# Kernel tuning notes

Hardware: AMD Instinct MI355X
Metric: run time of the kernel (lower is better)

The kernel has to match this reference:

```python
import jax, jax.numpy as jnp
import numpy as np

SUPPORT = 7
NEIGHBOR = 10
EPS = 1e-12
BN_EPS = 1e-5


def knn(v, k):
    # v: (b, n, 3) -> (b, n, k) indices of k nearest (excluding self)
    sq = jnp.sum(v * v, -1)
    d = sq[:, :, None] + sq[:, None, :] - 2.0 * jnp.einsum('bnd,bmd->bnm', v, v)
    _, idx = jax.lax.top_k(-d, k + 1)
    return idx[:, :, 1:]


def gather_nb(f, idx):
    # f: (b, n, c), idx: (b, m, k) -> (b, m, k, c)
    b = f.shape[0]
    return f[jnp.arange(b)[:, None, None], idx]


def nb_dir_norm(v, idx):
    d = gather_nb(v, idx) - v[:, :, None, :]
    n = jnp.linalg.norm(d, axis=-1, keepdims=True)
    return d / jnp.maximum(n, EPS)


def norm0(d):
    n = jnp.linalg.norm(d, axis=0, keepdims=True)
    return d / jnp.maximum(n, EPS)


def conv_surface(idx, v, directions, kernel_num):
    b, n, k = idx.shape
    dn = nb_dir_norm(v, idx)
    theta = jax.nn.relu(jnp.einsum('bnkd,de->bnke', dn, norm0(directions)))
    theta = theta.reshape(b, n, k, SUPPORT, kernel_num)
    return jnp.sum(jnp.max(theta, axis=2), axis=2)  # (b, n, kernel_num)


def conv_layer(idx, v, fmap, w, bias, directions, out_ch):
    b, n, k = idx.shape
    dn = nb_dir_norm(v, idx)
    theta = jax.nn.relu(jnp.einsum('bnkd,de->bnke', dn, norm0(directions)))  # (b,n,k,s*o)
    fout = fmap @ w + bias  # (b, n, (s+1)*o)
    center = fout[..., :out_ch]
    supp = gather_nb(fout[..., out_ch:], idx)  # (b, n, k, s*o)
    act = (theta * supp).reshape(b, n, k, SUPPORT, out_ch)
    return center + jnp.sum(jnp.max(act, axis=2), axis=2)


def pool(v, f, rate, nbn, seed):
    b, n, _ = v.shape
    idx = knn(v, nbn)
    pf = jnp.max(gather_nb(f, idx), axis=2)
    m = n // rate
    samp = jax.random.permutation(jax.random.key(seed), n)[:m]
    return v[:, samp, :], pf[:, samp, :]


def nearest_idx(tgt, src):
    d = (jnp.sum(src * src, -1)[:, None, :] + jnp.sum(tgt * tgt, -1)[:, :, None]
         - 2.0 * jnp.einsum('btd,bsd->bts', tgt, src))
    return jnp.argmin(d, axis=-1)  # (b, nt)


def bn(x, g, b_, m, var):
    # per-channel over last dim (torch BN1d after transpose)
    return (x - m) / jnp.sqrt(var + BN_EPS) * g + b_


def setup_inputs() -> dict:
    key = jax.random.key(0)
    ks = jax.random.split(key, 32)
    bs, n = 4, 2048
    d = {}
    d['vertices'] = jax.random.normal(ks[0], (bs, n, 3), jnp.float32)
    d['rgb_f'] = jax.random.normal(ks[1], (bs, 32, n), jnp.float32)
    d['dir0'] = jax.random.normal(ks[2], (3, SUPPORT * 64), jnp.float32)
    def conv_params(i, cin, cout):
        s = 1.0 / np.sqrt(cin)
        w = jax.random.uniform(ks[i], (cin, (SUPPORT + 1) * cout), jnp.float32, -s, s)
        b = jax.random.uniform(ks[i + 1], ((SUPPORT + 1) * cout,), jnp.float32, -s, s)
        dr = jax.random.normal(ks[i + 2], (3, SUPPORT * cout), jnp.float32)
        return w, b, dr
    d['w1'], d['b1'], d['d1'] = conv_params(3, 128, 128)
    d['w2'], d['b2'], d['d2'] = conv_params(6, 128, 256)
    d['w3'], d['b3'], d['d3'] = conv_params(9, 256, 256)
    d['w4'], d['b4'], d['d4'] = conv_params(12, 256, 512)
    d['rgb_w'] = jax.random.normal(ks[15], (64, 32), jnp.float32) * 0.1
    d['rgb_b'] = jnp.zeros((64,), jnp.float32)
    for nm, c in [('rbn', 64), ('bn1', 128), ('bn2', 256), ('bn3', 256)]:
        d[nm + '_g'] = jnp.ones((c,), jnp.float32)
        d[nm + '_b'] = jnp.zeros((c,), jnp.float32)
        d[nm + '_m'] = jnp.zeros((c,), jnp.float32)
        d[nm + '_v'] = jnp.ones((c,), jnp.float32)
    return d


def reference(vertices, rgb_f, dir0,
              w1, b1, d1, w2, b2, d2, w3, b3, d3, w4, b4, d4,
              rgb_w, rgb_b,
              rbn_g, rbn_b, rbn_m, rbn_v,
              bn1_g, bn1_b, bn1_m, bn1_v,
              bn2_g, bn2_b, bn2_m, bn2_v,
              bn3_g, bn3_b, bn3_m, bn3_v):
    bs, n, _ = vertices.shape
    idx = knn(vertices, NEIGHBOR)
    fm0 = jax.nn.relu(conv_surface(idx, vertices, dir0, 64))  # (b, n, 64)
    # rgb_conv_1: Conv1d(32,64,1) -> ReLU -> BN
    rgb = jax.nn.relu(jnp.einsum('oc,bcn->bno', rgb_w, rgb_f) + rgb_b)  # (b, n, 64)
    rgb = bn(rgb, rbn_g, rbn_b, rbn_m, rbn_v)
    fm0 = jnp.concatenate([fm0, rgb], axis=-1)  # (b, n, 128)
    fm1 = jax.nn.relu(bn(conv_layer(idx, vertices, fm0, w1, b1, d1, 128),
                         bn1_g, bn1_b, bn1_m, bn1_v))
    v1, fp1 = pool(vertices, fm1, 4, 4, 1)  # (b, n/4, ...)
    k1 = min(NEIGHBOR, v1.shape[1] // 8)
    idx1 = knn(v1, k1)
    fm2 = jax.nn.relu(bn(conv_layer(idx1, v1, fp1, w2, b2, d2, 256),
                         bn2_g, bn2_b, bn2_m, bn2_v))
    fm3 = jax.nn.relu(bn(conv_layer(idx1, v1, fm2, w3, b3, d3, 256),
                         bn3_g, bn3_b, bn3_m, bn3_v))
    v2, fp2 = pool(v1, fm3, 4, 4, 2)  # (b, n/16, ...)
    k2 = min(NEIGHBOR, v2.shape[1] // 8)
    idx2 = knn(v2, k2)
    fm4 = conv_layer(idx2, v2, fp2, w4, b4, d4, 512)
    f_global = jnp.max(fm4, axis=1)  # (b, 512)
    ni1 = nearest_idx(vertices, v1)  # (b, n)
    ni2 = nearest_idx(vertices, v2)
    ar = jnp.arange(bs)[:, None]
    fm2u = fm2[ar, ni1]
    fm3u = fm3[ar, ni1]
    fm4u = fm4[ar, ni2]
    feat = jnp.concatenate([fm0, fm1, fm2u, fm3u, fm4u], axis=2)  # (b, n, 1280)
    fuse = jnp.concatenate([feat, jnp.broadcast_to(f_global[:, None, :], (bs, n, 512))], axis=2)
    return feat.transpose(0, 2, 1), fuse.transpose(0, 2, 1)
```

## Files before the change

kernel.cpp:

```cpp
#include <hip/hip_runtime.h>
#include <hip/hip_bf16.h>
#include <math.h>

#define NB 10
#define KNN_K 11

typedef __attribute__((ext_vector_type(8))) short bf16x8;
typedef __attribute__((ext_vector_type(4))) float f32x4;

__device__ __forceinline__ float toF(float x) { return x; }
__device__ __forceinline__ float toF(__hip_bfloat16 x) { return __bfloat162float(x); }

__device__ __forceinline__ void tf2x32(unsigned k0, unsigned k1, unsigned& x0, unsigned& x1) {
  unsigned ks0 = k0, ks1 = k1, ks2 = k0 ^ k1 ^ 0x1BD11BDAu;
  x0 += ks0; x1 += ks1;
#define TF_R(r) { x0 += x1; x1 = (x1 << (r)) | (x1 >> (32 - (r))); x1 ^= x0; }
  TF_R(13) TF_R(15) TF_R(26) TF_R(6)  x0 += ks1; x1 += ks2 + 1u;
  TF_R(17) TF_R(29) TF_R(16) TF_R(24) x0 += ks2; x1 += ks0 + 2u;
  TF_R(13) TF_R(15) TF_R(26) TF_R(6)  x0 += ks0; x1 += ks1 + 3u;
  TF_R(17) TF_R(29) TF_R(16) TF_R(24) x0 += ks1; x1 += ks2 + 4u;
  TF_R(13) TF_R(15) TF_R(26) TF_R(6)  x0 += ks2; x1 += ks0 + 5u;
#undef TF_R
}

__device__ __forceinline__ unsigned long long shfl_xor_u64(unsigned long long v, int m) {
  unsigned lo = (unsigned)v, hi = (unsigned)(v >> 32);
  lo = (unsigned)__shfl_xor((int)lo, m);
  hi = (unsigned)__shfl_xor((int)hi, m);
  return ((unsigned long long)hi << 32) | lo;
}

__device__ __forceinline__ void knn_wave_body(const float4* __restrict__ pts, int N, int qi,
                                              int lane, int* __restrict__ o) {
  float4 p = pts[qi];
  float bd[KNN_K]; int bi[KNN_K];
#pragma unroll
  for (int t = 0; t < KNN_K; ++t) { bd[t] = 3.4e38f; bi[t] = 0x7fffffff; }
  for (int j = lane; j < N; j += 64) {
    float4 q = pts[j];
    float dot = p.x * q.x + p.y * q.y + p.z * q.z;
    float d = p.w + q.w - 2.0f * dot;
    if (d < bd[KNN_K - 1]) {
      float cd = d; int ci = j;
#pragma unroll
      for (int t = 0; t < KNN_K; ++t) {
        bool sw = cd < bd[t];
        float td = bd[t]; int ti = bi[t];
        bd[t] = sw ? cd : td; bi[t] = sw ? ci : ti;
        cd = sw ? td : cd;   ci = sw ? ti : ci;
      }
    }
  }
  int ptr = 0;
#pragma unroll 1
  for (int t = 0; t < KNN_K; ++t) {
    float d = 3.4e38f; int idx = 0x7fffffff;
#pragma unroll
    for (int s = 0; s < KNN_K; ++s) {
      bool sel = (s == ptr);
      d = sel ? bd[s] : d;
      idx = sel ? bi[s] : idx;
    }
    float rd = d; int ridx = idx;
#pragma unroll
    for (int s = 32; s > 0; s >>= 1) {
      float od = __shfl_xor(rd, s);
      int oi = __shfl_xor(ridx, s);
      if (od < rd || (od == rd && oi < ridx)) { rd = od; ridx = oi; }
    }
    if (d == rd && idx == ridx) ptr++;
    if (t >= 1 && lane == 0) o[t - 1] = ridx;
  }
}

__global__ __launch_bounds__(1024) void setup_kernel(
    const float* __restrict__ w1, __hip_bfloat16* __restrict__ o1,
    const float* __restrict__ w2, __hip_bfloat16* __restrict__ o2,
    const float* __restrict__ w3, __hip_bfloat16* __restrict__ o3,
    const float* __restrict__ w4, __hip_bfloat16* __restrict__ o4,
    const float* __restrict__ s0, float* __restrict__ n0,
    const float* __restrict__ s1, float* __restrict__ n1,
    const float* __restrict__ s2, float* __restrict__ n2,
    const float* __restrict__ s3, float* __restrict__ n3,
    const float* __restrict__ s4, float* __restrict__ n4,
    int* __restrict__ samp1, int* __restrict__ samp2,
    const float* __restrict__ v, int* __restrict__ idx0) {
  __shared__ __align__(16) char smem[49152];
  int bid = blockIdx.x;
  if (bid < 480) {
    int sub = threadIdx.x >> 8, t = threadIdx.x & 255;
    int wtile = bid * 4 + sub;
    float (*tbuf)[33] = (float(*)[33])(smem + sub * (32 * 33 * 4));
    const float* W; __hip_bfloat16* O; int K, N;
    if (wtile < 128)      { W = w1; O = o1; K = 128; N = 1024; }
    else if (wtile < 384) { wtile -= 128; W = w2; O = o2; K = 128; N = 2048; }
    else if (wtile < 896) { wtile -= 384; W = w3; O = o3; K = 256; N = 2048; }
    else                  { wtile -= 896; W = w4; O = o4; K = 256; N = 4096; }
    int tpr = N / 32;
    int tk = wtile / tpr, tn = wtile % tpr;
    int tx = t & 31, ty = t >> 5;
#pragma unroll
    for (int i = 0; i < 4; ++i)
      tbuf[ty + 8 * i][tx] = W[(size_t)(tk * 32 + ty + 8 * i) * N + tn * 32 + tx];
    __syncthreads();
#pragma unroll
    for (int i = 0; i < 4; ++i)
      O[(size_t)(tn * 32 + ty + 8 * i) * K + tk * 32 + tx] = __float2bfloat16(tbuf[tx][ty + 8 * i]);
    return;
  }
  if (bid < 489) {
    int e = (bid - 480) * 1024 + threadIdx.x;
    const float* S; float* D; int W;
    if (e < 448)                          { S = s0; D = n0; W = 448; }
    else if (e < 448 + 896)               { e -= 448; S = s1; D = n1; W = 896; }
    else if (e < 448 + 896 + 1792)        { e -= 448 + 896; S = s2; D = n2; W = 1792; }
    else if (e < 448 + 896 + 3584)        { e -= 448 + 896 + 1792; S = s3; D = n3; W = 1792; }
    else if (e < 448 + 896 + 3584 + 3584) { e -= 448 + 896 + 3584; S = s4; D = n4; W = 3584; }
    else return;
    float a = S[e], b = S[W + e], c = S[2 * W + e];
    float nr = fmaxf(sqrtf(a * a + b * b + c * c), 1e-12f);
    D[e] = a / nr; D[W + e] = b / nr; D[2 * W + e] = c / nr;
    return;
  }
  if (bid < 491) {
    unsigned long long (*buf)[2048] = (unsigned long long(*)[2048])smem;
    unsigned (*perm)[2048] = (unsigned(*)[2048])(smem + 32768);
    int which = bid - 489;
    int n = (which == 0) ? 2048 : 512;
    int m = (which == 0) ? 512 : 128;
    int R = (which == 0) ? 2 : 1;
    unsigned k0 = 0u, k1 = (which == 0) ? 1u : 2u;
    int* out = (which == 0) ? samp1 : samp2;
    int T = n >> 1;
    int t = threadIdx.x;
    bool act = (t < T);
    int pb = 0;
    unsigned valA = 0, valB = 0;
    int lb = 0;
    for (int r = 0; r < R; ++r) {
      unsigned a0 = 0u, a1 = 0u, ss0 = 0u, ss1 = 1u;
      tf2x32(k0, k1, a0, a1);
      tf2x32(k0, k1, ss0, ss1);
      unsigned long long kA = 0, kB = 0;
      if (act) {
        unsigned y0 = 0u, y1 = (unsigned)t;
        tf2x32(ss0, ss1, y0, y1);
        kA = ((unsigned long long)(y0 ^ y1) << 32) | (unsigned)t;
        y0 = 0u; y1 = (unsigned)(t + T);
        tf2x32(ss0, ss1, y0, y1);
        kB = ((unsigned long long)(y0 ^ y1) << 32) | (unsigned)(t + T);
      }
      for (int kk = 2; kk <= n; kk <<= 1) {
        for (int j = kk >> 1; j > 0; j >>= 1) {
          if (j == T) {
            if (act) {
              unsigned long long lo = (kA < kB) ? kA : kB;
              unsigned long long hi = (kA < kB) ? kB : kA;
              kA = lo; kB = hi;
            }
          } else if (j >= 64) {
            if (act) { buf[lb][t] = kA; buf[lb][t + T] = kB; }
            __syncthreads();
            if (act) {
              unsigned long long okA = buf[lb][t ^ j];
              unsigned long long okB = buf[lb][(t ^ j) + T];
              bool lower = ((t & j) == 0);
              bool upA = ((t & kk) == 0);
              bool upB = (((t + T) & kk) == 0);
              kA = (upA == lower) ? (kA < okA ? kA : okA) : (kA < okA ? okA : kA);
              kB = (upB == lower) ? (kB < okB ? kB : okB) : (kB < okB ? okB : kB);
            }
            lb ^= 1;
          } else {
            unsigned long long okA = shfl_xor_u64(kA, j);
            unsigned long long okB = shfl_xor_u64(kB, j);
            if (act) {
              bool lower = ((t & j) == 0);
              bool upA = ((t & kk) == 0);
              bool upB = (((t + T) & kk) == 0);
              kA = (upA == lower) ? (kA < okA ? kA : okA) : (kA < okA ? okA : kA);
              kB = (upB == lower) ? (kB < okB ? kB : okB) : (kB < okB ? okB : kB);
            }
          }
        }
      }
      if (act) {
        unsigned posA = (unsigned)(kA & 0xffffffffu);
        unsigned posB = (unsigned)(kB & 0xffffffffu);
        if (r == 0) { valA = posA; valB = posB; }
        else        { valA = perm[pb][posA]; valB = perm[pb][posB]; }
      }
      if (r + 1 < R) {
        __syncthreads();
        if (act) { perm[pb ^ 1][t] = valA; perm[pb ^ 1][t + T] = valB; }
        pb ^= 1;
        __syncthreads();
      }
      k0 = a0; k1 = a1;
    }
    if (t < m) out[t] = (int)valA;
    return;
  }
  {
    float4* pts = (float4*)smem;
    int i = bid - 491;
    int b = i >> 7, x = i & 127;
    const int N = 2048;
    const float* vb = v + (size_t)b * N * 3;
    for (int i2 = threadIdx.x; i2 < N; i2 += 1024) {
      float xx = vb[i2 * 3], yy = vb[i2 * 3 + 1], zz = vb[i2 * 3 + 2];
      pts[i2] = make_float4(xx, yy, zz, xx * xx + yy * yy + zz * zz);
    }
    __syncthreads();
    int wave = threadIdx.x >> 6;
    int lane = threadIdx.x & 63;
    int qi = x * 16 + wave;
    knn_wave_body(pts, N, qi, lane, idx0 + ((size_t)b * N + qi) * NB);
  }
}

__global__ __launch_bounds__(1024) void knn_wave_kernel(const float* __restrict__ v, int N,
                                                        int* __restrict__ out) {
  __shared__ float4 pts[2048];
  int b = blockIdx.y;
  const float* vb = v + (size_t)b * N * 3;
  for (int i = threadIdx.x; i < N; i += blockDim.x) {
    float x = vb[i * 3], y = vb[i * 3 + 1], z = vb[i * 3 + 2];
    pts[i] = make_float4(x, y, z, x * x + y * y + z * z);
  }
  __syncthreads();
  int qpb = blockDim.x >> 6;
  int wave = threadIdx.x >> 6;
  int lane = threadIdx.x & 63;
  int qi = blockIdx.x * qpb + wave;
  knn_wave_body(pts, N, qi, lane, out + ((size_t)b * N + qi) * NB);
}

__global__ __launch_bounds__(256) void fm0n_kernel(const float* __restrict__ v, const int* __restrict__ idx,
                                                   const float* __restrict__ dir0n,
                                                   const float* __restrict__ rgb_f, const float* __restrict__ w,
                                                   const float* __restrict__ bias, const float* __restrict__ g,
                                                   const float* __restrict__ bb, const float* __restrict__ mm,
                                                   const float* __restrict__ vv,
                                                   const int* __restrict__ samp1, const int* __restrict__ samp2,
                                                   float* __restrict__ fm0, __hip_bfloat16* __restrict__ fm0b,
                                                   int* __restrict__ ni1, int* __restrict__ ni2) {
  int z = blockIdx.z;
  int b = blockIdx.y;
  int tid = threadIdx.x;
  if (z >= 1) {
    __shared__ float4 sp[512];
    int S = (z == 1) ? 512 : 128;
    int* outp = (z == 1) ? ni1 : ni2;
    for (int i = tid; i < S; i += blockDim.x) {
      int src = (z == 1) ? samp1[i] : samp1[samp2[i]];
      const float* q = v + ((size_t)b * 2048 + src) * 3;
      float x = q[0], y = q[1], zz = q[2];
      sp[i] = make_float4(x, y, zz, x * x + y * y + zz * zz);
    }
    __syncthreads();
    int wave = tid >> 6, lane = tid & 63;
    int n = blockIdx.x * 4 + wave;
    const float* t = v + ((size_t)b * 2048 + n) * 3;
    float x = t[0], y = t[1], zz = t[2];
    float sqt = x * x + y * y + zz * zz;
    float best = 3.4e38f; int bi = 0x7fffffff;
    for (int s = lane; s < S; s += 64) {
      float4 q = sp[s];
      float d = q.w + sqt - 2.f * (x * q.x + y * q.y + zz * q.z);
      if (d < best) { best = d; bi = s; }
    }
#pragma unroll
    for (int m = 32; m > 0; m >>= 1) {
      float od = __shfl_xor(best, m);
      int oi = __shfl_xor(bi, m);
      if (od < best || (od == best && oi < bi)) { best = od; bi = oi; }
    }
    if (lane == 0) outp[(size_t)b * 2048 + n] = bi;
    return;
  }
  __shared__ float dn[4][NB][3];
  int n0 = blockIdx.x * 4;
  if (tid < 4 * NB) {
    int p = tid / NB, k = tid % NB;
    size_t row = (size_t)b * 2048 + (n0 + p);
    const float* c = v + row * 3;
    int nb = idx[row * NB + k];
    const float* q = v + ((size_t)b * 2048 + nb) * 3;
    float dx = q[0] - c[0], dy = q[1] - c[1], dz = q[2] - c[2];
    float nr = fmaxf(sqrtf(dx * dx + dy * dy + dz * dz), 1e-12f);
    dn[p][k][0] = dx / nr; dn[p][k][1] = dy / nr; dn[p][k][2] = dz / nr;
  }
  __syncthreads();
  int p = tid >> 6, c = tid & 63;
  int n = n0 + p;
  float acc = 0.f;
  for (int s = 0; s < 7; ++s) {
    int e = s * 64 + c;
    float d0 = dir0n[e], d1 = dir0n[448 + e], d2 = dir0n[896 + e];
    float mx = 0.f;
#pragma unroll
    for (int k = 0; k < NB; ++k) {
      float t = dn[p][k][0] * d0 + dn[p][k][1] * d1 + dn[p][k][2] * d2;
      mx = fmaxf(mx, fmaxf(t, 0.f));
    }
    acc += mx;
  }
  acc = fmaxf(acc, 0.f);
  const float* f = rgb_f + (size_t)b * 32 * 2048;
  float a2 = bias[c];
  for (int cc = 0; cc < 32; ++cc) a2 += w[c * 32 + cc] * f[cc * 2048 + n];
  a2 = fmaxf(a2, 0.f);
  a2 = (a2 - mm[c]) / sqrtf(vv[c] + 1e-5f) * g[c] + bb[c];
  size_t o = ((size_t)b * 2048 + n) * 128;
  fm0[o + c] = acc;
  fm0[o + 64 + c] = a2;
  fm0b[o + c] = __float2bfloat16(acc);
  fm0b[o + 64 + c] = __float2bfloat16(a2);
}

__global__ __launch_bounds__(256) void mfma_gemm_kernel(const __hip_bfloat16* __restrict__ A,
                                                        const __hip_bfloat16* __restrict__ BT,
                                                        const float* __restrict__ bias,
                                                        float* __restrict__ C,
                                                        __hip_bfloat16* __restrict__ Cb,
                                                        int M, int K, int N) {
  __shared__ __hip_bfloat16 Al[128 * 32];
  __shared__ __hip_bfloat16 Bl[128 * 32];
  int t = threadIdx.x;
  int l = t & 63;
  int w = t >> 6;
  int wm = w >> 1, wn = w & 1;
  int m0 = blockIdx.y * 128, n0 = blockIdx.x * 128;
  f32x4 zero = {0.f, 0.f, 0.f, 0.f};
  f32x4 acc[4][4];
#pragma unroll
  for (int i = 0; i < 4; ++i)
#pragma unroll
    for (int j = 0; j < 4; ++j) acc[i][j] = zero;

  for (int kt = 0; kt < K; kt += 32) {
#pragma unroll
    for (int j = 0; j < 2; ++j) {
      int c = t + 256 * j;
      int r = c >> 2, o = c & 3;
      *(uint4*)&Al[r * 32 + o * 8] = *(const uint4*)&A[(size_t)(m0 + r) * K + kt + o * 8];
      *(uint4*)&Bl[r * 32 + o * 8] = *(const uint4*)&BT[(size_t)(n0 + r) * K + kt + o * 8];
    }
    __syncthreads();
    bf16x8 af[4], bfv[4];
#pragma unroll
    for (int f = 0; f < 4; ++f) {
      af[f]  = *(const bf16x8*)&Al[(wm * 64 + f * 16 + (l & 15)) * 32 + (l >> 4) * 8];
      bfv[f] = *(const bf16x8*)&Bl[(wn * 64 + f * 16 + (l & 15)) * 32 + (l >> 4) * 8];
    }
#pragma unroll
    for (int i = 0; i < 4; ++i)
#pragma unroll
      for (int j = 0; j < 4; ++j)
        acc[i][j] = __builtin_amdgcn_mfma_f32_16x16x32_bf16(af[i], bfv[j], acc[i][j], 0, 0, 0);
    __syncthreads();
  }
  int col_l = l & 15, rbase = (l >> 4) * 4;
#pragma unroll
  for (int i = 0; i < 4; ++i) {
#pragma unroll
    for (int j = 0; j < 4; ++j) {
      int col = n0 + wn * 64 + j * 16 + col_l;
      float bv = bias[col];
#pragma unroll
      for (int r = 0; r < 4; ++r) {
        int m = m0 + wm * 64 + i * 16 + rbase + r;
        float val = acc[i][j][r] + bv;
        if (C)  C[(size_t)m * N + col] = val;
        if (Cb) Cb[(size_t)m * N + col] = __float2bfloat16(val);
      }
    }
  }
}

template <typename T>
__global__ __launch_bounds__(256) void conv_combine3_kernel(
    const int* __restrict__ idx, const float* __restrict__ v,
    const T* __restrict__ fout, const float* __restrict__ dirn,
    const float* __restrict__ g, const float* __restrict__ bb,
    const float* __restrict__ mm, const float* __restrict__ vv,
    int use_bn_relu, float* __restrict__ outf, __hip_bfloat16* __restrict__ outb,
    int Np, int Cout) {
  __shared__ float dnS[2][NB][3];
  __shared__ int nbS[2][NB];
  int b = blockIdx.y;
  int tid = threadIdx.x;
  int base = blockIdx.x * 256;
  int p0 = base / Cout;
  int nPts = (Cout < 256) ? 2 : 1;
  if (tid < nPts * NB) {
    int p = tid / NB, k = tid - p * NB;
    size_t prow = (size_t)b * Np + p0 + p;
    int nb = idx[prow * NB + k];
    const float* cpt = v + prow * 3;
    const float* q = v + ((size_t)b * Np + nb) * 3;
    float dx = q[0] - cpt[0], dy = q[1] - cpt[1], dz = q[2] - cpt[2];
    float nr = fmaxf(sqrtf(dx * dx + dy * dy + dz * dz), 1e-12f);
    dnS[p][k][0] = dx / nr; dnS[p][k][1] = dy / nr; dnS[p][k][2] = dz / nr;
    nbS[p][k] = b * Np + nb;
  }
  __syncthreads();
  int gid = base + tid;
  int n = gid / Cout, c = gid - n * Cout;
  int lp = n - p0;
  size_t row = (size_t)b * Np + n;
  float dn0[NB], dn1[NB], dn2[NB]; int nbr[NB];
#pragma unroll
  for (int k = 0; k < NB; ++k) {
    dn0[k] = dnS[lp][k][0]; dn1[k] = dnS[lp][k][1]; dn2[k] = dnS[lp][k][2];
    nbr[k] = nbS[lp][k];
  }
  int F = 8 * Cout, W7 = 7 * Cout;
  float acc = toF(fout[row * (size_t)F + c]);
  for (int s = 0; s < 7; ++s) {
    int e = s * Cout + c;
    float d0 = dirn[e], d1 = dirn[W7 + e], d2 = dirn[2 * W7 + e];
    float mx = -3.4e38f;
#pragma unroll
    for (int k = 0; k < NB; ++k) {
      float t = fmaxf(dn0[k] * d0 + dn1[k] * d1 + dn2[k] * d2, 0.f);
      float sv = toF(fout[(size_t)nbr[k] * F + Cout + e]);
      mx = fmaxf(mx, t * sv);
    }
    acc += mx;
  }
  if (use_bn_relu) {
    acc = (acc - mm[c]) / sqrtf(vv[c] + 1e-5f) * g[c] + bb[c];
    acc = fmaxf(acc, 0.f);
  }
  outf[row * (size_t)Cout + c] = acc;
  if (outb) outb[row * (size_t)Cout + c] = __float2bfloat16(acc);
}

__global__ void pool_kernel(const float* __restrict__ v, const float* __restrict__ fm,
                            const int* __restrict__ idx10, const int* __restrict__ samp,
                            float* __restrict__ v_out, float* __restrict__ f_out,
                            __hip_bfloat16* __restrict__ f_out_b, int Nin, int C) {
  int b = blockIdx.y, mi = blockIdx.x, c = threadIdx.x;
  int n = samp[mi];
  size_t row = (size_t)b * Nin + n;
  float mx = -3.4e38f;
#pragma unroll
  for (int j = 0; j < 4; ++j) {
    int nb = idx10[row * NB + j];
    mx = fmaxf(mx, fm[((size_t)b * Nin + nb) * C + c]);
  }
  int Mout = gridDim.x;
  f_out[((size_t)b * Mout + mi) * C + c] = mx;
  f_out_b[((size_t)b * Mout + mi) * C + c] = __float2bfloat16(mx);
  if (c < 3) v_out[((size_t)b * Mout + mi) * 3 + c] = v[row * 3 + c];
}

__global__ __launch_bounds__(256) void output3_kernel(
    const float* __restrict__ fm0, const float* __restrict__ fm1,
    const float* __restrict__ fm2, const float* __restrict__ fm3,
    const float* __restrict__ fm4,
    const int* __restrict__ ni1, const int* __restrict__ ni2,
    float* __restrict__ out) {
  __shared__ float tile[64][33];
  __shared__ int srow[64];
  int b = blockIdx.z;
  int cc0 = blockIdx.y * 32;
  int n0 = blockIdx.x * 64;
  int tid = threadIdx.x;
  float* out0 = out;
  float* out1 = out + (size_t)4 * 1280 * 2048;
  if (cc0 >= 1280) {
    __shared__ float red[8][32];
    __shared__ float fgv[32];
    int coff = cc0 - 1280;
    int tx = tid & 31, ty = tid >> 5;
    float pm = -3.4e38f;
    for (int p = ty; p < 128; p += 8)
      pm = fmaxf(pm, fm4[((size_t)b * 128 + p) * 512 + coff + tx]);
    red[ty][tx] = pm;
    __syncthreads();
    if (tid < 32) {
      float m = red[0][tid];
#pragma unroll
      for (int r = 1; r < 8; ++r) m = fmaxf(m, red[r][tid]);
      fgv[tid] = m;
    }
    __syncthreads();
    int lx = tid & 63, ly = tid >> 6;
#pragma unroll
    for (int ci = 0; ci < 8; ++ci) {
      int cl = ly + 4 * ci;
      out1[((size_t)b * 1792 + cc0 + cl) * 2048 + n0 + lx] = fgv[cl];
    }
    return;
  }
  const float* P; int Cs, coff, mode;
  if (cc0 < 128)       { P = fm0; Cs = 128; coff = cc0;        mode = 0; }
  else if (cc0 < 256)  { P = fm1; Cs = 128; coff = cc0 - 128;  mode = 0; }
  else if (cc0 < 512)  { P = fm2; Cs = 256; coff = cc0 - 256;  mode = 1; }
  else if (cc0 < 768)  { P = fm3; Cs = 256; coff = cc0 - 512;  mode = 1; }
  else                 { P = fm4; Cs = 512; coff = cc0 - 768;  mode = 2; }
  if (tid < 64) {
    int n = n0 + tid;
    size_t r2 = (size_t)b * 2048 + n;
    int sr;
    if (mode == 0)      sr = b * 2048 + n;
    else if (mode == 1) sr = b * 512 + ni1[r2];
    else                sr = b * 128 + ni2[r2];
    srow[tid] = sr;
  }
  __syncthreads();
  int tx = tid & 31, ty = tid >> 5;
#pragma unroll
  for (int r = 0; r < 8; ++r) {
    int nl = ty + 8 * r;
    tile[nl][tx] = P[(size_t)srow[nl] * Cs + coff + tx];
  }
  __syncthreads();
  int lx = tid & 63, ly = tid >> 6;
#pragma unroll
  for (int ci = 0; ci < 8; ++ci) {
    int cl = ly + 4 * ci;
    int cc = cc0 + cl;
    float vv = tile[lx][cl];
    out1[((size_t)b * 1792 + cc) * 2048 + n0 + lx] = vv;
    out0[((size_t)b * 1280 + cc) * 2048 + n0 + lx] = vv;
  }
}

extern "C" void kernel_launch(void* const* d_in, const int* in_sizes, int n_in,
                              void* d_out, int out_size, void* d_ws, size_t ws_size,
                              hipStream_t stream) {
  (void)in_sizes; (void)n_in; (void)out_size; (void)ws_size;
  const float* vertices = (const float*)d_in[0];
  const float* rgb_f    = (const float*)d_in[1];
  const float* dir0     = (const float*)d_in[2];
  const float* w1 = (const float*)d_in[3],  *b1 = (const float*)d_in[4],  *d1 = (const float*)d_in[5];
  const float* w2 = (const float*)d_in[6],  *b2 = (const float*)d_in[7],  *d2 = (const float*)d_in[8];
  const float* w3 = (const float*)d_in[9],  *b3 = (const float*)d_in[10], *d3 = (const float*)d_in[11];
  const float* w4 = (const float*)d_in[12], *b4 = (const float*)d_in[13], *d4 = (const float*)d_in[14];
  const float* rgb_w = (const float*)d_in[15], *rgb_b = (const float*)d_in[16];
  const float* rbn_g = (const float*)d_in[17], *rbn_b = (const float*)d_in[18];
  const float* rbn_m = (const float*)d_in[19], *rbn_v = (const float*)d_in[20];
  const float* bn1_g = (const float*)d_in[21], *bn1_b = (const float*)d_in[22];
  const float* bn1_m = (const float*)d_in[23], *bn1_v = (const float*)d_in[24];
  const float* bn2_g = (const float*)d_in[25], *bn2_b = (const float*)d_in[26];
  const float* bn2_m = (const float*)d_in[27], *bn2_v = (const float*)d_in[28];
  const float* bn3_g = (const float*)d_in[29], *bn3_b = (const float*)d_in[30];
  const float* bn3_m = (const float*)d_in[31], *bn3_v = (const float*)d_in[32];
  float* out = (float*)d_out;

  char* ws = (char*)d_ws;
  size_t off = 0;
  auto alloc = [&](size_t bytes) -> void* {
    void* p = ws + off;
    off += (bytes + 255) & ~(size_t)255;
    return p;
  };
  int*   samp1 = (int*)alloc(512 * 4);
  int*   samp2 = (int*)alloc(128 * 4);
  int*   idx0  = (int*)alloc((size_t)4 * 2048 * NB * 4);
  int*   idx1  = (int*)alloc((size_t)4 * 512 * NB * 4);
  int*   idx2  = (int*)alloc((size_t)4 * 128 * NB * 4);
  float* fm0   = (float*)alloc((size_t)4 * 2048 * 128 * 4);
  float* fm1   = (float*)alloc((size_t)4 * 2048 * 128 * 4);
  float* fout  = (float*)alloc((size_t)4 * 2048 * 1024 * 4);
  __hip_bfloat16* foutb = (__hip_bfloat16*)alloc((size_t)4 * 2048 * 1024 * 2);
  float* v1    = (float*)alloc((size_t)4 * 512 * 3 * 4);
  float* fp1   = (float*)alloc((size_t)4 * 512 * 128 * 4);
  float* fm2   = (float*)alloc((size_t)4 * 512 * 256 * 4);
  float* fm3   = (float*)alloc((size_t)4 * 512 * 256 * 4);
  float* v2    = (float*)alloc((size_t)4 * 128 * 3 * 4);
  float* fp2   = (float*)alloc((size_t)4 * 128 * 256 * 4);
  float* fm4   = (float*)alloc((size_t)4 * 128 * 512 * 4);
  int*   ni1   = (int*)alloc((size_t)4 * 2048 * 4);
  int*   ni2   = (int*)alloc((size_t)4 * 2048 * 4);
  __hip_bfloat16* fm0b = (__hip_bfloat16*)alloc((size_t)4 * 2048 * 128 * 2);
  __hip_bfloat16* fp1b = (__hip_bfloat16*)alloc((size_t)4 * 512 * 128 * 2);
  __hip_bfloat16* fm2b = (__hip_bfloat16*)alloc((size_t)4 * 512 * 256 * 2);
  __hip_bfloat16* fp2b = (__hip_bfloat16*)alloc((size_t)4 * 128 * 256 * 2);
  __hip_bfloat16* wt1  = (__hip_bfloat16*)alloc((size_t)1024 * 128 * 2);
  __hip_bfloat16* wt2  = (__hip_bfloat16*)alloc((size_t)2048 * 128 * 2);
  __hip_bfloat16* wt3  = (__hip_bfloat16*)alloc((size_t)2048 * 256 * 2);
  __hip_bfloat16* wt4  = (__hip_bfloat16*)alloc((size_t)4096 * 256 * 2);
  float* d0n = (float*)alloc((size_t)3 * 448 * 4);
  float* d1n = (float*)alloc((size_t)3 * 896 * 4);
  float* d2n = (float*)alloc((size_t)3 * 1792 * 4);
  float* d3n = (float*)alloc((size_t)3 * 1792 * 4);
  float* d4n = (float*)alloc((size_t)3 * 3584 * 4);

  setup_kernel<<<1003, 1024, 0, stream>>>(w1, wt1, w2, wt2, w3, wt3, w4, wt4,
                                          dir0, d0n, d1, d1n, d2, d2n, d3, d3n, d4, d4n,
                                          samp1, samp2, vertices, idx0);

  fm0n_kernel<<<dim3(512, 4, 3), 256, 0, stream>>>(vertices, idx0, d0n, rgb_f, rgb_w, rgb_b,
                                                   rbn_g, rbn_b, rbn_m, rbn_v, samp1, samp2,
                                                   fm0, fm0b, ni1, ni2);

  mfma_gemm_kernel<<<dim3(1024 / 128, 8192 / 128), 256, 0, stream>>>(fm0b, wt1, b1, nullptr, foutb, 8192, 128, 1024);
  conv_combine3_kernel<__hip_bfloat16><<<dim3(2048 * 128 / 256, 4), 256, 0, stream>>>(idx0, vertices, foutb, d1n,
      bn1_g, bn1_b, bn1_m, bn1_v, 1, fm1, nullptr, 2048, 128);

  pool_kernel<<<dim3(512, 4), 128, 0, stream>>>(vertices, fm1, idx0, samp1, v1, fp1, fp1b, 2048, 128);
  knn_wave_kernel<<<dim3(512 / 4, 4), 256, 0, stream>>>(v1, 512, idx1);

  mfma_gemm_kernel<<<dim3(2048 / 128, 2048 / 128), 256, 0, stream>>>(fp1b, wt2, b2, nullptr, foutb, 2048, 128, 2048);
  conv_combine3_kernel<__hip_bfloat16><<<dim3(512 * 256 / 256, 4), 256, 0, stream>>>(idx1, v1, foutb, d2n,
      bn2_g, bn2_b, bn2_m, bn2_v, 1, fm2, fm2b, 512, 256);
  mfma_gemm_kernel<<<dim3(2048 / 128, 2048 / 128), 256, 0, stream>>>(fm2b, wt3, b3, nullptr, foutb, 2048, 256, 2048);
  conv_combine3_kernel<__hip_bfloat16><<<dim3(512 * 256 / 256, 4), 256, 0, stream>>>(idx1, v1, foutb, d3n,
      bn3_g, bn3_b, bn3_m, bn3_v, 1, fm3, nullptr, 512, 256);

  pool_kernel<<<dim3(128, 4), 256, 0, stream>>>(v1, fm3, idx1, samp2, v2, fp2, fp2b, 512, 256);
  knn_wave_kernel<<<dim3(128 / 4, 4), 256, 0, stream>>>(v2, 128, idx2);

  mfma_gemm_kernel<<<dim3(4096 / 128, 512 / 128), 256, 0, stream>>>(fp2b, wt4, b4, fout, nullptr, 512, 256, 4096);
  conv_combine3_kernel<float><<<dim3(128 * 512 / 256, 4), 256, 0, stream>>>(idx2, v2, fout, d4n,
      nullptr, nullptr, nullptr, nullptr, 0, fm4, nullptr, 128, 512);

  output3_kernel<<<dim3(32, 56, 4), 256, 0, stream>>>(fm0, fm1, fm2, fm3, fm4, ni1, ni2, out);
}
```

Baseline: 245.9 us.

## Replace single-block bitonic permutation sort with multi-block rank-counting

The random permutation used for sampling was computed by one or two blocks running a serial bitonic sort with many barriers, which could become the critical path of the setup kernel. It is now computed by 17 blocks that each rank a chunk of keys by counting smaller keys, scattering each index to its rank position. The two-round permutation for the first pool is kept as two separate permutations composed at lookup time (p1a[p1b[i]]). This adds O(n^2) comparisons and an extra indirection in the consumers, in exchange for far more parallelism and fewer barriers.

```diff
diff --git a/kernel.cpp b/kernel.cpp
--- a/kernel.cpp
+++ b/kernel.cpp
@@ -7,6 +7,7 @@
 
 typedef __attribute__((ext_vector_type(8))) short bf16x8;
 typedef __attribute__((ext_vector_type(4))) float f32x4;
+typedef unsigned long long ull;
 
 __device__ __forceinline__ float toF(float x) { return x; }
 __device__ __forceinline__ float toF(__hip_bfloat16 x) { return __bfloat162float(x); }
@@ -23,13 +24,6 @@
 #undef TF_R
 }
 
-__device__ __forceinline__ unsigned long long shfl_xor_u64(unsigned long long v, int m) {
-  unsigned lo = (unsigned)v, hi = (unsigned)(v >> 32);
-  lo = (unsigned)__shfl_xor((int)lo, m);
-  hi = (unsigned)__shfl_xor((int)hi, m);
-  return ((unsigned long long)hi << 32) | lo;
-}
-
 __device__ __forceinline__ void knn_wave_body(const float4* __restrict__ pts, int N, int qi,
                                               int lane, int* __restrict__ o) {
   float4 p = pts[qi];
@@ -83,7 +77,7 @@
     const float* __restrict__ s2, float* __restrict__ n2,
     const float* __restrict__ s3, float* __restrict__ n3,
     const float* __restrict__ s4, float* __restrict__ n4,
-    int* __restrict__ samp1, int* __restrict__ samp2,
+    int* __restrict__ p1a, int* __restrict__ p1b, int* __restrict__ samp2,
     const float* __restrict__ v, int* __restrict__ idx0) {
   __shared__ __align__(16) char smem[49152];
   int bid = blockIdx.x;
@@ -122,88 +116,43 @@
     D[e] = a / nr; D[W + e] = b / nr; D[2 * W + e] = c / nr;
     return;
   }
-  if (bid < 491) {
-    unsigned long long (*buf)[2048] = (unsigned long long(*)[2048])smem;
-    unsigned (*perm)[2048] = (unsigned(*)[2048])(smem + 32768);
-    int which = bid - 489;
-    int n = (which == 0) ? 2048 : 512;
-    int m = (which == 0) ? 512 : 128;
-    int R = (which == 0) ? 2 : 1;
-    unsigned k0 = 0u, k1 = (which == 0) ? 1u : 2u;
-    int* out = (which == 0) ? samp1 : samp2;
-    int T = n >> 1;
-    int t = threadIdx.x;
-    bool act = (t < T);
-    int pb = 0;
-    unsigned valA = 0, valB = 0;
-    int lb = 0;
-    for (int r = 0; r < R; ++r) {
-      unsigned a0 = 0u, a1 = 0u, ss0 = 0u, ss1 = 1u;
-      tf2x32(k0, k1, a0, a1);
-      tf2x32(k0, k1, ss0, ss1);
-      unsigned long long kA = 0, kB = 0;
-      if (act) {
-        unsigned y0 = 0u, y1 = (unsigned)t;
-        tf2x32(ss0, ss1, y0, y1);
-        kA = ((unsigned long long)(y0 ^ y1) << 32) | (unsigned)t;
-        y0 = 0u; y1 = (unsigned)(t + T);
-        tf2x32(ss0, ss1, y0, y1);
-        kB = ((unsigned long long)(y0 ^ y1) << 32) | (unsigned)(t + T);
-      }
-      for (int kk = 2; kk <= n; kk <<= 1) {
-        for (int j = kk >> 1; j > 0; j >>= 1) {
-          if (j == T) {
-            if (act) {
-              unsigned long long lo = (kA < kB) ? kA : kB;
-              unsigned long long hi = (kA < kB) ? kB : kA;
-              kA = lo; kB = hi;
-            }
-          } else if (j >= 64) {
-            if (act) { buf[lb][t] = kA; buf[lb][t + T] = kB; }
-            __syncthreads();
-            if (act) {
-              unsigned long long okA = buf[lb][t ^ j];
-              unsigned long long okB = buf[lb][(t ^ j) + T];
-              bool lower = ((t & j) == 0);
-              bool upA = ((t & kk) == 0);
-              bool upB = (((t + T) & kk) == 0);
-              kA = (upA == lower) ? (kA < okA ? kA : okA) : (kA < okA ? okA : kA);
-              kB = (upB == lower) ? (kB < okB ? kB : okB) : (kB < okB ? okB : kB);
-            }
-            lb ^= 1;
-          } else {
-            unsigned long long okA = shfl_xor_u64(kA, j);
-            unsigned long long okB = shfl_xor_u64(kB, j);
-            if (act) {
-              bool lower = ((t & j) == 0);
-              bool upA = ((t & kk) == 0);
-              bool upB = (((t + T) & kk) == 0);
-              kA = (upA == lower) ? (kA < okA ? kA : okA) : (kA < okA ? okA : kA);
-              kB = (upB == lower) ? (kB < okB ? kB : okB) : (kB < okB ? okB : kB);
-            }
-          }
-        }
-      }
-      if (act) {
-        unsigned posA = (unsigned)(kA & 0xffffffffu);
-        unsigned posB = (unsigned)(kB & 0xffffffffu);
-        if (r == 0) { valA = posA; valB = posB; }
-        else        { valA = perm[pb][posA]; valB = perm[pb][posB]; }
-      }
-      if (r + 1 < R) {
-        __syncthreads();
-        if (act) { perm[pb ^ 1][t] = valA; perm[pb ^ 1][t + T] = valB; }
-        pb ^= 1;
-        __syncthreads();
-      }
-      k0 = a0; k1 = a1;
-    }
-    if (t < m) out[t] = (int)valA;
+  if (bid < 506) {
+    ull* keys = (ull*)smem;
+    int which, chunk;
+    if (bid < 497)      { which = 0; chunk = bid - 489; }
+    else if (bid < 505) { which = 1; chunk = bid - 497; }
+    else                { which = 2; chunk = 0; }
+    unsigned mk0, mk1;
+    if (which == 0)      { mk0 = 0u; mk1 = 1u; }
+    else if (which == 1) { unsigned a0 = 0u, a1 = 0u; tf2x32(0u, 1u, a0, a1); mk0 = a0; mk1 = a1; }
+    else                 { mk0 = 0u; mk1 = 2u; }
+    unsigned sk0 = 0u, sk1 = 1u;
+    tf2x32(mk0, mk1, sk0, sk1);
+    int n = (which == 2) ? 512 : 2048;
+    int* outp = (which == 0) ? p1a : (which == 1) ? p1b : samp2;
+    for (int i = threadIdx.x; i < n; i += 1024) {
+      unsigned y0 = 0u, y1 = (unsigned)i;
+      tf2x32(sk0, sk1, y0, y1);
+      keys[i] = ((ull)(y0 ^ y1) << 32) | (unsigned)i;
+    }
+    __syncthreads();
+    int rpb = (which == 2) ? 512 : 256;
+    int tpr = 1024 / rpb;
+    int row = chunk * rpb + (int)(threadIdx.x / tpr);
+    int sub = threadIdx.x % tpr;
+    int seg = n / tpr;
+    ull my = keys[row];
+    int cnt = 0;
+    for (int j = sub * seg; j < (sub + 1) * seg; ++j) cnt += (keys[j] < my) ? 1 : 0;
+#pragma unroll
+    for (int m = 1; m < 4; m <<= 1)
+      if (m < tpr) cnt += __shfl_xor(cnt, m);
+    if (sub == 0) outp[cnt] = row;
     return;
   }
   {
     float4* pts = (float4*)smem;
-    int i = bid - 491;
+    int i = bid - 506;
     int b = i >> 7, x = i & 127;
     const int N = 2048;
     const float* vb = v + (size_t)b * N * 3;
@@ -242,7 +191,8 @@
                                                    const float* __restrict__ bias, const float* __restrict__ g,
                                                    const float* __restrict__ bb, const float* __restrict__ mm,
                                                    const float* __restrict__ vv,
-                                                   const int* __restrict__ samp1, const int* __restrict__ samp2,
+                                                   const int* __restrict__ p1a, const int* __restrict__ p1b,
+                                                   const int* __restrict__ samp2,
                                                    float* __restrict__ fm0, __hip_bfloat16* __restrict__ fm0b,
                                                    int* __restrict__ ni1, int* __restrict__ ni2) {
   int z = blockIdx.z;
@@ -253,7 +203,7 @@
     int S = (z == 1) ? 512 : 128;
     int* outp = (z == 1) ? ni1 : ni2;
     for (int i = tid; i < S; i += blockDim.x) {
-      int src = (z == 1) ? samp1[i] : samp1[samp2[i]];
+      int src = (z == 1) ? p1a[p1b[i]] : p1a[p1b[samp2[i]]];
       const float* q = v + ((size_t)b * 2048 + src) * 3;
       float x = q[0], y = q[1], zz = q[2];
       sp[i] = make_float4(x, y, zz, x * x + y * y + zz * zz);
@@ -439,11 +389,12 @@
 }
 
 __global__ void pool_kernel(const float* __restrict__ v, const float* __restrict__ fm,
-                            const int* __restrict__ idx10, const int* __restrict__ samp,
+                            const int* __restrict__ idx10,
+                            const int* __restrict__ sampA, const int* __restrict__ sampB,
                             float* __restrict__ v_out, float* __restrict__ f_out,
                             __hip_bfloat16* __restrict__ f_out_b, int Nin, int C) {
   int b = blockIdx.y, mi = blockIdx.x, c = threadIdx.x;
-  int n = samp[mi];
+  int n = sampB ? sampA[sampB[mi]] : sampA[mi];
   size_t row = (size_t)b * Nin + n;
   float mx = -3.4e38f;
 #pragma unroll
@@ -559,8 +510,9 @@
     off += (bytes + 255) & ~(size_t)255;
     return p;
   };
-  int*   samp1 = (int*)alloc(512 * 4);
-  int*   samp2 = (int*)alloc(128 * 4);
+  int*   p1a   = (int*)alloc(2048 * 4);
+  int*   p1b   = (int*)alloc(2048 * 4);
+  int*   samp2 = (int*)alloc(512 * 4);
   int*   idx0  = (int*)alloc((size_t)4 * 2048 * NB * 4);
   int*   idx1  = (int*)alloc((size_t)4 * 512 * NB * 4);
   int*   idx2  = (int*)alloc((size_t)4 * 128 * NB * 4);
@@ -591,19 +543,19 @@
   float* d3n = (float*)alloc((size_t)3 * 1792 * 4);
   float* d4n = (float*)alloc((size_t)3 * 3584 * 4);
 
-  setup_kernel<<<1003, 1024, 0, stream>>>(w1, wt1, w2, wt2, w3, wt3, w4, wt4,
+  setup_kernel<<<1018, 1024, 0, stream>>>(w1, wt1, w2, wt2, w3, wt3, w4, wt4,
                                           dir0, d0n, d1, d1n, d2, d2n, d3, d3n, d4, d4n,
-                                          samp1, samp2, vertices, idx0);
+                                          p1a, p1b, samp2, vertices, idx0);
 
   fm0n_kernel<<<dim3(512, 4, 3), 256, 0, stream>>>(vertices, idx0, d0n, rgb_f, rgb_w, rgb_b,
-                                                   rbn_g, rbn_b, rbn_m, rbn_v, samp1, samp2,
+                                                   rbn_g, rbn_b, rbn_m, rbn_v, p1a, p1b, samp2,
                                                    fm0, fm0b, ni1, ni2);
 
   mfma_gemm_kernel<<<dim3(1024 / 128, 8192 / 128), 256, 0, stream>>>(fm0b, wt1, b1, nullptr, foutb, 8192, 128, 1024);
   conv_combine3_kernel<__hip_bfloat16><<<dim3(2048 * 128 / 256, 4), 256, 0, stream>>>(idx0, vertices, foutb, d1n,
       bn1_g, bn1_b, bn1_m, bn1_v, 1, fm1, nullptr, 2048, 128);
 
-  pool_kernel<<<dim3(512, 4), 128, 0, stream>>>(vertices, fm1, idx0, samp1, v1, fp1, fp1b, 2048, 128);
+  pool_kernel<<<dim3(512, 4), 128, 0, stream>>>(vertices, fm1, idx0, p1a, p1b, v1, fp1, fp1b, 2048, 128);
   knn_wave_kernel<<<dim3(512 / 4, 4), 256, 0, stream>>>(v1, 512, idx1);
 
   mfma_gemm_kernel<<<dim3(2048 / 128, 2048 / 128), 256, 0, stream>>>(fp1b, wt2, b2, nullptr, foutb, 2048, 128, 2048);
@@ -613,7 +565,7 @@
   conv_combine3_kernel<__hip_bfloat16><<<dim3(512 * 256 / 256, 4), 256, 0, stream>>>(idx1, v1, foutb, d3n,
       bn3_g, bn3_b, bn3_m, bn3_v, 1, fm3, nullptr, 512, 256);
 
-  pool_kernel<<<dim3(128, 4), 256, 0, stream>>>(v1, fm3, idx1, samp2, v2, fp2, fp2b, 512, 256);
+  pool_kernel<<<dim3(128, 4), 256, 0, stream>>>(v1, fm3, idx1, samp2, nullptr, v2, fp2, fp2b, 512, 256);
   knn_wave_kernel<<<dim3(128 / 4, 4), 256, 0, stream>>>(v2, 128, idx2);
 
   mfma_gemm_kernel<<<dim3(4096 / 128, 512 / 128), 256, 0, stream>>>(fp2b, wt4, b4, fout, nullptr, 512, 256, 4096);
```

Measured after the change: 247.8 us. No clear change (+0.7%).
